# Kernel optimization log

Measured on AMD Instinct MI355X. Metric: run time of the kernel, lower is better.

## Reference

```python
import jax, jax.numpy as jnp
import numpy as np

EPS = 1e-7  # tf.keras.backend.epsilon()
R_ITER = 3

def squash(v, axis=-1):
    # Eq.(1): scale = |s|^2 / (1+|s|^2) / |s|
    s2 = jnp.sum(v * v, axis=axis, keepdims=True)
    scale = s2 / (1.0 + s2) / jnp.sqrt(s2 + EPS)
    return scale * v

def setup_inputs() -> dict:
    key = jax.random.key(0)
    k1, k2 = jax.random.split(key)
    B, Ni, Di = 64, 1152, 8
    No, Do = 64, 16
    inputs = jax.random.normal(k1, (B, Ni, Di), dtype=jnp.float32)
    # W init: tf.random.normal(stddev=0.1)
    W = 0.1 * jax.random.normal(k2, (1, Ni, No, Do, Di), dtype=jnp.float32)
    return {"inputs": inputs, "W": W}

def reference(inputs, W):
    B, Ni, Di = inputs.shape
    No, Do = W.shape[2], W.shape[3]
    # inputs_hat[b,i,o,d] = W[i,o,d,k] @ inputs[b,i,k]  (tile+matmul fused)
    u_hat = jnp.einsum('iodk,bik->biod', W[0], inputs)  # [B,Ni,No,Do]
    # raw routing logits start at shape [1,Ni,No]; broadcast to [B,...] on first update
    b_logits = jnp.zeros((1, Ni, No), dtype=inputs.dtype)
    for it in range(R_ITER):
        c = jax.nn.softmax(b_logits, axis=2)            # over output caps
        s = jnp.sum(c[..., None] * u_hat, axis=1, keepdims=True)  # [B,1,No,Do]
        v = squash(s, axis=-1)                          # [B,1,No,Do]
        if it < R_ITER - 1:
            # agreement: <u_hat, v> over capsule dim
            b_logits = b_logits + jnp.sum(u_hat * v, axis=-1)  # [B,Ni,No]
    out = jnp.squeeze(v, axis=1)                        # [B,No,Do]
    routing_weights = c[..., None, None]                # [B,Ni,No,1,1] as in TF
    return out, routing_weights
```

## Files before the change

### kernel.cpp

```cpp
#include <hip/hip_runtime.h>


#define B_      64
#define NI_     1152
#define DI_     8
#define NO_     64
#define DO_     16
#define NOD_    1024
#define CH_     96
#define CI_     12
#define BG_     8
#define BSPLIT_ 8
#define V_ELEMS 65536
#define PADR    33

static_assert(CH_ * CI_ == NI_, "chunking");
static_assert(BG_ * BSPLIT_ == B_, "b split");

template <int MODE>
__global__ __launch_bounds__(256, 3)
void caps_pass(const float* __restrict__ X,
               const float* __restrict__ W,
               const float* __restrict__ vin,
               float* __restrict__ part,
               float* __restrict__ rw)
{
    __shared__ float  x_lds[BG_][CI_ * DI_];
    __shared__ float4 wtile[NO_ * PADR];
    __shared__ float  e_lds[BG_][NO_];
    __shared__ float  invS[BG_];

    const int t  = threadIdx.x;
    const int o  = t >> 2, q = t & 3;
    const int ch = blockIdx.x;
    const int b0 = blockIdx.y * BG_;
    const int i0 = ch * CI_;

    for (int f = t; f < BG_ * CI_ * DI_ / 4; f += 256) {
        int bb = f / (CI_ * DI_ / 4), r = f - bb * (CI_ * DI_ / 4);
        ((float4*)x_lds)[f] =
            ((const float4*)(X + ((size_t)(b0 + bb) * NI_ + i0) * DI_))[r];
    }
    float vreg[BG_][4];
    if (MODE >= 1) {
#pragma unroll
        for (int b = 0; b < BG_; ++b) {
            float4 qv = *((const float4*)(vin + (size_t)(b0 + b) * NOD_ + 4 * t));
            vreg[b][0]=qv.x; vreg[b][1]=qv.y; vreg[b][2]=qv.z; vreg[b][3]=qv.w;
        }
    }
    __syncthreads();

    float acc[BG_][4];
#pragma unroll
    for (int b = 0; b < BG_; ++b) { acc[b][0]=0.f; acc[b][1]=0.f; acc[b][2]=0.f; acc[b][3]=0.f; }

    const float4* Wq = (const float4*)W;

    for (int ci = 0; ci < CI_; ++ci) {
        const int i = i0 + ci;

        const float4* wg = Wq + (size_t)i * 2048;
        float4 tmp[8];
#pragma unroll
        for (int j = 0; j < 8; ++j) tmp[j] = wg[t + 256 * j];
#pragma unroll
        for (int j = 0; j < 8; ++j) {
            const int f = t + 256 * j;
            wtile[(f >> 5) * PADR + (f & 31)] = tmp[j];
        }
        __syncthreads();

        float wf[4][8];
#pragma unroll
        for (int jj = 0; jj < 4; ++jj) {
            float4 a0 = wtile[o * PADR + (4 * q + jj) * 2];
            float4 a1 = wtile[o * PADR + (4 * q + jj) * 2 + 1];
            wf[jj][0]=a0.x; wf[jj][1]=a0.y; wf[jj][2]=a0.z; wf[jj][3]=a0.w;
            wf[jj][4]=a1.x; wf[jj][5]=a1.y; wf[jj][6]=a1.z; wf[jj][7]=a1.w;
        }

        float u[BG_][4];
#pragma unroll
        for (int b = 0; b < BG_; ++b) {
            const float* xb = &x_lds[b][ci * DI_];
            const float x0=xb[0],x1=xb[1],x2=xb[2],x3=xb[3];
            const float x4=xb[4],x5=xb[5],x6=xb[6],x7=xb[7];
#pragma unroll
            for (int jj = 0; jj < 4; ++jj) {
                float s = wf[jj][0] * x0;
                s = fmaf(wf[jj][1], x1, s); s = fmaf(wf[jj][2], x2, s);
                s = fmaf(wf[jj][3], x3, s); s = fmaf(wf[jj][4], x4, s);
                s = fmaf(wf[jj][5], x5, s); s = fmaf(wf[jj][6], x6, s);
                s = fmaf(wf[jj][7], x7, s);
                u[b][jj] = s;
            }
            if (MODE >= 1) {
                float a = u[b][0]*vreg[b][0] + u[b][1]*vreg[b][1]
                        + u[b][2]*vreg[b][2] + u[b][3]*vreg[b][3];
                a += __shfl_xor(a, 1);
                a += __shfl_xor(a, 2);
                if (q == 0) e_lds[b][o] = __expf(a);
            } else {
                acc[b][0]+=u[b][0]; acc[b][1]+=u[b][1];
                acc[b][2]+=u[b][2]; acc[b][3]+=u[b][3];
            }
        }

        if (MODE >= 1) {
            __syncthreads();
            {
                const int bb = t >> 5, l = t & 31;
                float s = e_lds[bb][l] + e_lds[bb][l + 32];
                s += __shfl_xor(s, 1);  s += __shfl_xor(s, 2);  s += __shfl_xor(s, 4);
                s += __shfl_xor(s, 8);  s += __shfl_xor(s, 16);
                if (l == 0) invS[bb] = 1.0f / s;
            }
            __syncthreads();
#pragma unroll
            for (int b = 0; b < BG_; ++b) {
                const float c = e_lds[b][o] * invS[b];
                acc[b][0] = fmaf(c, u[b][0], acc[b][0]);
                acc[b][1] = fmaf(c, u[b][1], acc[b][1]);
                acc[b][2] = fmaf(c, u[b][2], acc[b][2]);
                acc[b][3] = fmaf(c, u[b][3], acc[b][3]);
                if (MODE == 2 && q == 0)
                    rw[((size_t)(b0 + b) * NI_ + i) * NO_ + o] = c;
            }
        } else {
            __syncthreads();
        }
    }

#pragma unroll
    for (int b = 0; b < BG_; ++b) {
        float4 val;
        val.x=acc[b][0]; val.y=acc[b][1]; val.z=acc[b][2]; val.w=acc[b][3];
        *((float4*)(part + (((size_t)(b0 + b) * CH_ + ch) * NOD_ + 4 * t))) = val;
    }
}

template <int MODE>
__global__ __launch_bounds__(128)
void caps_squash(const float* __restrict__ part, const float* __restrict__ v0in,
                 float* __restrict__ vout)
{
    const int c4 = blockIdx.x * 128 + threadIdx.x;
    const int b = c4 >> 8, od4 = c4 & 255;
    const float4* p = (const float4*)part + (size_t)b * CH_ * 256 + od4;
    float4 s = {0.f, 0.f, 0.f, 0.f};
#pragma unroll 8
    for (int ch = 0; ch < CH_; ++ch) {
        float4 q = p[(size_t)ch * 256];
        s.x += q.x; s.y += q.y; s.z += q.z; s.w += q.w;
    }
    if (MODE == 0) { s.x*=(1.f/64.f); s.y*=(1.f/64.f); s.z*=(1.f/64.f); s.w*=(1.f/64.f); }
    float s2 = s.x*s.x + s.y*s.y + s.z*s.z + s.w*s.w;
    s2 += __shfl_xor(s2, 1); s2 += __shfl_xor(s2, 2);
    const float scale = s2 / ((1.0f + s2) * sqrtf(s2 + 1e-7f));
    float4 v; v.x = scale*s.x; v.y = scale*s.y; v.z = scale*s.z; v.w = scale*s.w;
    if (MODE == 1) {
        float4 v0 = ((const float4*)v0in)[c4];
        v.x += v0.x; v.y += v0.y; v.z += v0.z; v.w += v0.w;
    }
    ((float4*)vout)[c4] = v;
}

__global__ __launch_bounds__(1024, 1)
void caps_naive(const float* __restrict__ X, const float* __restrict__ W,
                float* __restrict__ outv, float* __restrict__ outc)
{
    __shared__ float xs[NI_ * DI_];
    __shared__ float agree[NO_];
    __shared__ float expo[NO_];
    __shared__ float s2sh[NO_];
    __shared__ float den;

    const int b = blockIdx.x, tid = threadIdx.x;
    const int o = tid >> 4, d = tid & 15;

    for (int f = tid; f < NI_ * DI_; f += 1024)
        xs[f] = X[(size_t)b * NI_ * DI_ + f];
    __syncthreads();

    float vprev = 0.f, v0 = 0.f, vout = 0.f;
    for (int phase = 0; phase < 3; ++phase) {
        float sacc = 0.f;
        for (int i = 0; i < NI_; ++i) {
            const float* wp = W + (size_t)i * 8192 + (size_t)tid * 8;
            const float* xp = xs + i * DI_;
            float u = 0.f;
#pragma unroll
            for (int k = 0; k < 8; ++k) u = fmaf(wp[k], xp[k], u);
            if (phase == 0) { sacc += u; continue; }
            if (d == 0) agree[o] = 0.f;
            __syncthreads();
            atomicAdd(&agree[o], u * vprev);
            __syncthreads();
            if (tid == 0) den = 0.f;
            __syncthreads();
            if (d == 0) { float e = __expf(agree[o]); expo[o] = e; atomicAdd(&den, e); }
            __syncthreads();
            float c = expo[o] / den;
            sacc = fmaf(c, u, sacc);
            if (phase == 2 && d == 0)
                outc[((size_t)b * NI_ + i) * NO_ + o] = c;
            __syncthreads();
        }
        if (phase == 0) sacc *= (1.0f / 64.0f);
        if (d == 0) s2sh[o] = 0.f;
        __syncthreads();
        atomicAdd(&s2sh[o], sacc * sacc);
        __syncthreads();
        const float s2 = s2sh[o];
        const float scale = s2 / ((1.0f + s2) * sqrtf(s2 + 1e-7f));
        const float vv = scale * sacc;
        if (phase == 0)      { v0 = vv; vprev = vv; }
        else if (phase == 1) { vprev = v0 + vv; }
        else                 { vout = vv; }
        __syncthreads();
    }
    outv[(size_t)b * (NO_ * DO_) + tid] = vout;
}

extern "C" void kernel_launch(void* const* d_in, const int* in_sizes, int n_in,
                              void* d_out, int out_size, void* d_ws, size_t ws_size,
                              hipStream_t stream)
{
    const float *X, *W;
    if (in_sizes[0] < in_sizes[1]) { X = (const float*)d_in[0]; W = (const float*)d_in[1]; }
    else                           { X = (const float*)d_in[1]; W = (const float*)d_in[0]; }

    float* out  = (float*)d_out;
    float* outv = out;
    float* outc = out + V_ELEMS;

    const size_t needBig = ((size_t)B_ * CH_ * NOD_ + 2 * (size_t)B_ * NOD_) * sizeof(float);
    if (ws_size < needBig) {
        caps_naive<<<B_, 1024, 0, stream>>>(X, W, outv, outc);
        return;
    }

    float* part = (float*)d_ws;
    float* v0   = part + (size_t)B_ * CH_ * NOD_;
    float* w01  = v0 + (size_t)B_ * NOD_;

    dim3 gP(CH_, BSPLIT_), blk(256), gS(128), blkS(128);
    caps_pass<0><<<gP, blk, 0, stream>>>(X, W, nullptr, part, nullptr);
    caps_squash<0><<<gS, blkS, 0, stream>>>(part, nullptr, v0);
    caps_pass<1><<<gP, blk, 0, stream>>>(X, W, v0, part, nullptr);
    caps_squash<1><<<gS, blkS, 0, stream>>>(part, v0, w01);
    caps_pass<2><<<gP, blk, 0, stream>>>(X, W, w01, part, outc);
    caps_squash<2><<<gS, blkS, 0, stream>>>(part, nullptr, outv);
}
```

Before: 229.7 us.

## Add LDS-free first routing pass and prefetch next W tile in routing passes

Adds a dedicated caps_pass0 kernel for the first iteration that reads each thread's W rows straight from global memory into registers. It skips the LDS transpose tile and all per-capsule barriers, and allows 4 blocks per CU. The softmax passes now issue the global loads for the next input capsule's W tile before the current capsule's math. This lets global memory latency overlap with compute, at the cost of extra live registers. Pass 0's direct W loads are strided per thread, so coalescing may be worse than the tiled load.

```diff
diff --git a/kernel.cpp b/kernel.cpp
--- a/kernel.cpp
+++ b/kernel.cpp
@@ -17,6 +17,66 @@
 static_assert(CH_ * CI_ == NI_, "chunking");
 static_assert(BG_ * BSPLIT_ == B_, "b split");
 
+__global__ __launch_bounds__(256, 4)
+void caps_pass0(const float* __restrict__ X,
+                const float* __restrict__ W,
+                float* __restrict__ part)
+{
+    __shared__ float x_lds[BG_][CI_ * DI_];
+
+    const int t  = threadIdx.x;
+    const int ch = blockIdx.x;
+    const int b0 = blockIdx.y * BG_;
+    const int i0 = ch * CI_;
+
+    for (int f = t; f < BG_ * CI_ * DI_ / 4; f += 256) {
+        int bb = f / (CI_ * DI_ / 4), r = f - bb * (CI_ * DI_ / 4);
+        ((float4*)x_lds)[f] =
+            ((const float4*)(X + ((size_t)(b0 + bb) * NI_ + i0) * DI_))[r];
+    }
+    __syncthreads();
+
+    float acc[BG_][4];
+#pragma unroll
+    for (int b = 0; b < BG_; ++b) { acc[b][0]=0.f; acc[b][1]=0.f; acc[b][2]=0.f; acc[b][3]=0.f; }
+
+    const float4* Wq = (const float4*)W;
+
+    for (int ci = 0; ci < CI_; ++ci) {
+        const int i = i0 + ci;
+        const float4* wp = Wq + (size_t)i * 2048 + (size_t)t * 8;
+        float wf[4][8];
+#pragma unroll
+        for (int j = 0; j < 4; ++j) {
+            float4 q0 = wp[2*j], q1 = wp[2*j + 1];
+            wf[j][0]=q0.x; wf[j][1]=q0.y; wf[j][2]=q0.z; wf[j][3]=q0.w;
+            wf[j][4]=q1.x; wf[j][5]=q1.y; wf[j][6]=q1.z; wf[j][7]=q1.w;
+        }
+#pragma unroll
+        for (int b = 0; b < BG_; ++b) {
+            const float* xb = &x_lds[b][ci * DI_];
+            const float x0=xb[0],x1=xb[1],x2=xb[2],x3=xb[3];
+            const float x4=xb[4],x5=xb[5],x6=xb[6],x7=xb[7];
+#pragma unroll
+            for (int j = 0; j < 4; ++j) {
+                float s = wf[j][0] * x0;
+                s = fmaf(wf[j][1], x1, s); s = fmaf(wf[j][2], x2, s);
+                s = fmaf(wf[j][3], x3, s); s = fmaf(wf[j][4], x4, s);
+                s = fmaf(wf[j][5], x5, s); s = fmaf(wf[j][6], x6, s);
+                s = fmaf(wf[j][7], x7, s);
+                acc[b][j] += s;
+            }
+        }
+    }
+
+#pragma unroll
+    for (int b = 0; b < BG_; ++b) {
+        float4 val;
+        val.x=acc[b][0]; val.y=acc[b][1]; val.z=acc[b][2]; val.w=acc[b][3];
+        *((float4*)(part + (((size_t)(b0 + b) * CH_ + ch) * NOD_ + 4 * t))) = val;
+    }
+}
+
 template <int MODE>
 __global__ __launch_bounds__(256, 3)
 void caps_pass(const float* __restrict__ X,
@@ -42,28 +102,29 @@
             ((const float4*)(X + ((size_t)(b0 + bb) * NI_ + i0) * DI_))[r];
     }
     float vreg[BG_][4];
-    if (MODE >= 1) {
-#pragma unroll
-        for (int b = 0; b < BG_; ++b) {
-            float4 qv = *((const float4*)(vin + (size_t)(b0 + b) * NOD_ + 4 * t));
-            vreg[b][0]=qv.x; vreg[b][1]=qv.y; vreg[b][2]=qv.z; vreg[b][3]=qv.w;
-        }
+#pragma unroll
+    for (int b = 0; b < BG_; ++b) {
+        float4 qv = *((const float4*)(vin + (size_t)(b0 + b) * NOD_ + 4 * t));
+        vreg[b][0]=qv.x; vreg[b][1]=qv.y; vreg[b][2]=qv.z; vreg[b][3]=qv.w;
+    }
+
+    float acc[BG_][4];
+#pragma unroll
+    for (int b = 0; b < BG_; ++b) { acc[b][0]=0.f; acc[b][1]=0.f; acc[b][2]=0.f; acc[b][3]=0.f; }
+
+    const float4* Wq = (const float4*)W;
+
+    float4 tmp[8];
+    {
+        const float4* wg = Wq + (size_t)i0 * 2048;
+#pragma unroll
+        for (int j = 0; j < 8; ++j) tmp[j] = wg[t + 256 * j];
     }
     __syncthreads();
-
-    float acc[BG_][4];
-#pragma unroll
-    for (int b = 0; b < BG_; ++b) { acc[b][0]=0.f; acc[b][1]=0.f; acc[b][2]=0.f; acc[b][3]=0.f; }
-
-    const float4* Wq = (const float4*)W;
 
     for (int ci = 0; ci < CI_; ++ci) {
         const int i = i0 + ci;
 
-        const float4* wg = Wq + (size_t)i * 2048;
-        float4 tmp[8];
-#pragma unroll
-        for (int j = 0; j < 8; ++j) tmp[j] = wg[t + 256 * j];
 #pragma unroll
         for (int j = 0; j < 8; ++j) {
             const int f = t + 256 * j;
@@ -78,6 +139,12 @@
             float4 a1 = wtile[o * PADR + (4 * q + jj) * 2 + 1];
             wf[jj][0]=a0.x; wf[jj][1]=a0.y; wf[jj][2]=a0.z; wf[jj][3]=a0.w;
             wf[jj][4]=a1.x; wf[jj][5]=a1.y; wf[jj][6]=a1.z; wf[jj][7]=a1.w;
+        }
+
+        if (ci + 1 < CI_) {
+            const float4* wg = Wq + (size_t)(i + 1) * 2048;
+#pragma unroll
+            for (int j = 0; j < 8; ++j) tmp[j] = wg[t + 256 * j];
         }
 
         float u[BG_][4];
@@ -95,40 +162,31 @@
                 s = fmaf(wf[jj][7], x7, s);
                 u[b][jj] = s;
             }
-            if (MODE >= 1) {
-                float a = u[b][0]*vreg[b][0] + u[b][1]*vreg[b][1]
-                        + u[b][2]*vreg[b][2] + u[b][3]*vreg[b][3];
-                a += __shfl_xor(a, 1);
-                a += __shfl_xor(a, 2);
-                if (q == 0) e_lds[b][o] = __expf(a);
-            } else {
-                acc[b][0]+=u[b][0]; acc[b][1]+=u[b][1];
-                acc[b][2]+=u[b][2]; acc[b][3]+=u[b][3];
-            }
-        }
-
-        if (MODE >= 1) {
-            __syncthreads();
-            {
-                const int bb = t >> 5, l = t & 31;
-                float s = e_lds[bb][l] + e_lds[bb][l + 32];
-                s += __shfl_xor(s, 1);  s += __shfl_xor(s, 2);  s += __shfl_xor(s, 4);
-                s += __shfl_xor(s, 8);  s += __shfl_xor(s, 16);
-                if (l == 0) invS[bb] = 1.0f / s;
-            }
-            __syncthreads();
-#pragma unroll
-            for (int b = 0; b < BG_; ++b) {
-                const float c = e_lds[b][o] * invS[b];
-                acc[b][0] = fmaf(c, u[b][0], acc[b][0]);
-                acc[b][1] = fmaf(c, u[b][1], acc[b][1]);
-                acc[b][2] = fmaf(c, u[b][2], acc[b][2]);
-                acc[b][3] = fmaf(c, u[b][3], acc[b][3]);
-                if (MODE == 2 && q == 0)
-                    rw[((size_t)(b0 + b) * NI_ + i) * NO_ + o] = c;
-            }
-        } else {
-            __syncthreads();
+            float a = u[b][0]*vreg[b][0] + u[b][1]*vreg[b][1]
+                    + u[b][2]*vreg[b][2] + u[b][3]*vreg[b][3];
+            a += __shfl_xor(a, 1);
+            a += __shfl_xor(a, 2);
+            if (q == 0) e_lds[b][o] = __expf(a);
+        }
+
+        __syncthreads();
+        {
+            const int bb = t >> 5, l = t & 31;
+            float s = e_lds[bb][l] + e_lds[bb][l + 32];
+            s += __shfl_xor(s, 1);  s += __shfl_xor(s, 2);  s += __shfl_xor(s, 4);
+            s += __shfl_xor(s, 8);  s += __shfl_xor(s, 16);
+            if (l == 0) invS[bb] = 1.0f / s;
+        }
+        __syncthreads();
+#pragma unroll
+        for (int b = 0; b < BG_; ++b) {
+            const float c = e_lds[b][o] * invS[b];
+            acc[b][0] = fmaf(c, u[b][0], acc[b][0]);
+            acc[b][1] = fmaf(c, u[b][1], acc[b][1]);
+            acc[b][2] = fmaf(c, u[b][2], acc[b][2]);
+            acc[b][3] = fmaf(c, u[b][3], acc[b][3]);
+            if (MODE == 2 && q == 0)
+                rw[((size_t)(b0 + b) * NI_ + i) * NO_ + o] = c;
         }
     }
 
@@ -246,7 +304,7 @@
     float* w01  = v0 + (size_t)B_ * NOD_;
 
     dim3 gP(CH_, BSPLIT_), blk(256), gS(128), blkS(128);
-    caps_pass<0><<<gP, blk, 0, stream>>>(X, W, nullptr, part, nullptr);
+    caps_pass0<<<gP, blk, 0, stream>>>(X, W, part);
     caps_squash<0><<<gS, blkS, 0, stream>>>(part, nullptr, v0);
     caps_pass<1><<<gP, blk, 0, stream>>>(X, W, v0, part, nullptr);
     caps_squash<1><<<gS, blkS, 0, stream>>>(part, v0, w01);
```

Result: slower. 344.3 us (+49.9%).
